# Optimization experiments

Hardware: AMD Instinct MI355X
Metric: run time of the kernel (lower is better)

## Reference

```python
import jax, jax.numpy as jnp
import numpy as np

N_NODES = 50000
N_EDGES = 100000
N_RELS = 64
D_IN = 64
D_OUT = 64


def setup_inputs() -> dict:
    key = jax.random.key(0)
    k1, k2, k3, k4, k5, k6 = jax.random.split(key, 6)
    h = jax.random.normal(k1, (N_NODES, D_IN), dtype=jnp.float32)
    src = jax.random.randint(k2, (N_EDGES,), 0, N_NODES)
    rel = jax.random.randint(k3, (N_EDGES,), 0, N_RELS)
    dst = jax.random.randint(k4, (N_EDGES,), 0, N_NODES)
    edges = jnp.stack([src, rel, dst], axis=1)
    # xavier_uniform with gain for relu: bound = gain * sqrt(6 / (fan_in + fan_out))
    gain = float(np.sqrt(2.0))
    bound = gain * float(np.sqrt(6.0 / (D_IN + D_OUT)))
    weight = jax.random.uniform(k5, (N_RELS, D_IN, D_OUT), dtype=jnp.float32,
                                minval=-bound, maxval=bound)
    self_loop_weight = jax.random.uniform(k6, (D_IN, D_OUT), dtype=jnp.float32,
                                          minval=-bound, maxval=bound)
    return {"h": h, "edges": edges, "weight": weight,
            "self_loop_weight": self_loop_weight}


def reference(h, edges, weight, self_loop_weight):
    # h: (N, D_IN); edges: (E, 3) int columns (src, rel, dst)
    src, rel, dst = edges[:, 0], edges[:, 1], edges[:, 2]
    n_nodes = h.shape[0]
    n_edges = src.shape[0]

    # per-edge relation-specific transform: (E,1,in) bmm (E,in,out) -> (E,out)
    src_h = h[src]                                    # (E, D_IN)
    msg = jnp.einsum('ei,eio->eo', src_h, weight[rel])  # (E, D_OUT)

    # -> last edge index per destination node
    last_edge = jax.ops.segment_max(jnp.arange(n_edges, dtype=jnp.int32), dst,
                                    num_segments=n_nodes)  # (N,)
    # msg = msg[index_matrix[dst]]: every edge to node d takes the msg of the
    # last edge pointing to d
    msg = msg[last_edge[dst]]                          # (E, D_OUT)

    # scatter-mean aggregate over dst (only nodes with incoming edges updated)
    sums = jax.ops.segment_sum(msg, dst, num_segments=n_nodes)          # (N, D_OUT)
    counts = jax.ops.segment_sum(jnp.ones((n_edges,), h.dtype), dst,
                                 num_segments=n_nodes)                   # (N,)
    has_in = counts > 0
    agg = jnp.where(has_in[:, None],
                    sums / jnp.maximum(counts, 1.0)[:, None], 0.0)

    out = h @ self_loop_weight                         # (N, D_OUT)
    return out + agg
```

## Files before the change

### kernel.cpp

```cpp
#include <hip/hip_runtime.h>

#define NN 50000
#define NE 100000
#define NREL 64
#define D 64
#define RCAP 1280
#define SCAP 8192
#define CSTR 16
#define BR   8
#define SBLK 64
#define FILL_BLOCKS 128
#define FILL_ITERS  2

#define SC_BLK ((NE + 255) / 256)
#define TR_BLK 65
#define HC_BLK 160

typedef unsigned long long u64;
using f16x8 = __attribute__((ext_vector_type(8))) _Float16;
using f32x4 = __attribute__((ext_vector_type(4))) float;

#define WS_CURSOR  (400 * 1024)
#define WS_RBUCKET (408 * 1024)
#define WS_SBUCKET (736 * 1024)
#define WS_H2      (768 * 1024)
#define WS_WST     (7168 * 1024)
#define WS_W16T    (7176 * 1024)

struct H4 { _Float16 v[4]; };

__global__ __launch_bounds__(256) void k_init(u64* __restrict__ packed, int* __restrict__ cursor) {
    const int t = blockIdx.x * 256 + threadIdx.x;
    const int nthr = gridDim.x * 256;
    for (int i = t; i < NN; i += nthr) packed[i] = 0ull;
    if (t < 65) cursor[t * CSTR] = 0;
}

__global__ __launch_bounds__(256) void k_scatpre(
    const int* __restrict__ edges, const float* __restrict__ h,
    const float* __restrict__ weight, const float* __restrict__ wself,
    u64* __restrict__ packed, _Float16* __restrict__ h2,
    _Float16* __restrict__ w16T, _Float16* __restrict__ wsT)
{
    __shared__ _Float16 tile[D * D];

    if (blockIdx.x < SC_BLK) {
        const int e = blockIdx.x * 256 + threadIdx.x;
        if (e < NE) {
            const int s = edges[e * 3 + 0];
            const int r = edges[e * 3 + 1];
            const int d = edges[e * 3 + 2];
            const u64 key = ((u64)(e + 1) << 22) | ((u64)r << 16) | (u64)s;
            atomicMax(&packed[d], key);
        }
        return;
    }

    if (blockIdx.x < SC_BLK + TR_BLK) {
        const int r = blockIdx.x - SC_BLK;
        const float4* __restrict__ src4 = reinterpret_cast<const float4*>(
            (r < NREL) ? (weight + (size_t)r * D * D) : wself);
        #pragma unroll
        for (int it = 0; it < 4; ++it) {
            const int idx = it * 256 + threadIdx.x;
            const float4 w = src4[idx];
            const int k  = idx >> 4;
            const int n0 = (idx & 15) << 2;
            tile[(n0 + 0) * D + k] = (_Float16)w.x;
            tile[(n0 + 1) * D + k] = (_Float16)w.y;
            tile[(n0 + 2) * D + k] = (_Float16)w.z;
            tile[(n0 + 3) * D + k] = (_Float16)w.w;
        }
        __syncthreads();
        f16x8* __restrict__ dst = reinterpret_cast<f16x8*>(
            (r < NREL) ? (w16T + ((size_t)r << 12)) : wsT);
        const f16x8* __restrict__ src = reinterpret_cast<const f16x8*>(tile);
        #pragma unroll
        for (int it = 0; it < 2; ++it)
            dst[it * 256 + threadIdx.x] = src[it * 256 + threadIdx.x];
        return;
    }

    const int t = (blockIdx.x - SC_BLK - TR_BLK) * 256 + threadIdx.x;
    const int nthr = HC_BLK * 256;
    const float4* __restrict__ hf4 = reinterpret_cast<const float4*>(h);
    H4* __restrict__ o4 = reinterpret_cast<H4*>(h2);
    for (int m = t; m < NN * (D / 4); m += nthr) {
        const float4 p = hf4[m];
        H4 o;
        o.v[0] = (_Float16)p.x; o.v[1] = (_Float16)p.y;
        o.v[2] = (_Float16)p.z; o.v[3] = (_Float16)p.w;
        o4[m] = o;
    }
}

__global__ __launch_bounds__(256) void k_fill(
    const u64* __restrict__ packed, int* __restrict__ cursor,
    unsigned* __restrict__ rbucket, unsigned* __restrict__ sbucket)
{
    __shared__ int hcnt[65];
    __shared__ int hbase[65];
    const int t = threadIdx.x;
    if (t < 65) hcnt[t] = 0;
    __syncthreads();

    int      myr[FILL_ITERS];
    int      myslot[FILL_ITERS];
    unsigned myent[FILL_ITERS];

    #pragma unroll
    for (int it = 0; it < FILL_ITERS; ++it) {
        const int v = (blockIdx.x * FILL_ITERS + it) * 256 + t;
        myr[it] = -1;
        if (v < NN) {
            u64 key = packed[v];
            if (key) {
                myr[it]   = (int)((key >> 16) & 63);
                myent[it] = ((unsigned)v << 16) | (unsigned)(key & 0xFFFF);
            } else {
                myr[it]   = 64;
                myent[it] = (unsigned)v;
            }
            myslot[it] = atomicAdd(&hcnt[myr[it]], 1);
        }
    }
    __syncthreads();
    if (t < 65 && hcnt[t] > 0)
        hbase[t] = atomicAdd(&cursor[t * CSTR], hcnt[t]);
    __syncthreads();

    #pragma unroll
    for (int it = 0; it < FILL_ITERS; ++it) {
        const int r = myr[it];
        if (r >= 0) {
            const int p = hbase[r] + myslot[it];
            if (r < 64) { if (p < RCAP) rbucket[r * RCAP + p] = myent[it]; }
            else        { if (p < SCAP) sbucket[p] = myent[it]; }
        }
    }
}

__global__ __launch_bounds__(256) void k_compute(
    const _Float16* __restrict__ h2, const _Float16* __restrict__ w16T,
    const _Float16* __restrict__ wsT, const unsigned* __restrict__ rbucket,
    const unsigned* __restrict__ sbucket, const int* __restrict__ cursor,
    float* __restrict__ out)
{
    const int lane = threadIdx.x & 63;
    const int wv   = threadIdx.x >> 6;
    const bool isRel = blockIdx.x < NREL * BR;

    int r = 64, wslot, wstride, cnt;
    const unsigned* __restrict__ seg;
    if (isRel) {
        r = blockIdx.x / BR;
        wslot = (blockIdx.x % BR) * 4 + wv;
        wstride = BR * 4;
        seg = rbucket + r * RCAP;
        cnt = min(cursor[r * CSTR], RCAP);
    } else {
        wslot = (blockIdx.x - NREL * BR) * 4 + wv;
        wstride = SBLK * 4;
        seg = sbucket;
        cnt = min(cursor[64 * CSTR], SCAP);
    }
    if (cnt == 0 || wslot * 16 >= cnt) return;

    const int kbase = (lane >> 4) * 8;
    const int ncol  = lane & 15;

    f16x8 was[4][2];
    #pragma unroll
    for (int nt = 0; nt < 4; ++nt)
        #pragma unroll
        for (int ks = 0; ks < 2; ++ks)
            was[nt][ks] = *reinterpret_cast<const f16x8*>(
                wsT + (size_t)(nt * 16 + ncol) * D + ks * 32 + kbase);

    f16x8 wa[4][2];
    if (isRel) {
        const _Float16* __restrict__ wr = w16T + ((size_t)r << 12);
        #pragma unroll
        for (int nt = 0; nt < 4; ++nt)
            #pragma unroll
            for (int ks = 0; ks < 2; ++ks)
                wa[nt][ks] = *reinterpret_cast<const f16x8*>(
                    wr + (size_t)(nt * 16 + ncol) * D + ks * 32 + kbase);
    }

    for (int t = wslot; t * 16 < cnt; t += wstride) {
        const unsigned ent = seg[min(t * 16 + ncol, cnt - 1)];
        const int v = isRel ? (int)(ent >> 16) : (int)ent;
        const int s = (int)(ent & 0xFFFF);

        f32x4 c[4];
        #pragma unroll
        for (int nt = 0; nt < 4; ++nt) c[nt] = (f32x4){0.f, 0.f, 0.f, 0.f};

        {
            const f16x8 b0 = *reinterpret_cast<const f16x8*>(h2 + (size_t)v * D + kbase);
            const f16x8 b1 = *reinterpret_cast<const f16x8*>(h2 + (size_t)v * D + 32 + kbase);
            #pragma unroll
            for (int nt = 0; nt < 4; ++nt) {
                c[nt] = __builtin_amdgcn_mfma_f32_16x16x32_f16(was[nt][0], b0, c[nt], 0, 0, 0);
                c[nt] = __builtin_amdgcn_mfma_f32_16x16x32_f16(was[nt][1], b1, c[nt], 0, 0, 0);
            }
        }
        if (isRel) {
            const f16x8 b0 = *reinterpret_cast<const f16x8*>(h2 + (size_t)s * D + kbase);
            const f16x8 b1 = *reinterpret_cast<const f16x8*>(h2 + (size_t)s * D + 32 + kbase);
            #pragma unroll
            for (int nt = 0; nt < 4; ++nt) {
                c[nt] = __builtin_amdgcn_mfma_f32_16x16x32_f16(wa[nt][0], b0, c[nt], 0, 0, 0);
                c[nt] = __builtin_amdgcn_mfma_f32_16x16x32_f16(wa[nt][1], b1, c[nt], 0, 0, 0);
            }
        }

        float* __restrict__ orow = out + (size_t)v * D + (lane >> 4) * 4;
        #pragma unroll
        for (int nt = 0; nt < 4; ++nt) {
            *reinterpret_cast<float4*>(orow + nt * 16) =
                make_float4(c[nt][0], c[nt][1], c[nt][2], c[nt][3]);
        }
    }
}

extern "C" void kernel_launch(void* const* d_in, const int* in_sizes, int n_in,
                              void* d_out, int out_size, void* d_ws, size_t ws_size,
                              hipStream_t stream) {
    const float* h      = (const float*)d_in[0];
    const int*   edges  = (const int*)d_in[1];
    const float* weight = (const float*)d_in[2];
    const float* wself  = (const float*)d_in[3];
    float* out = (float*)d_out;

    char* ws = (char*)d_ws;
    u64*      packed  = (u64*)ws;
    int*      cursor  = (int*)(ws + WS_CURSOR);
    unsigned* rbucket = (unsigned*)(ws + WS_RBUCKET);
    unsigned* sbucket = (unsigned*)(ws + WS_SBUCKET);
    _Float16* h2      = (_Float16*)(ws + WS_H2);
    _Float16* wsT     = (_Float16*)(ws + WS_WST);
    _Float16* w16T    = (_Float16*)(ws + WS_W16T);

    k_init<<<98, 256, 0, stream>>>(packed, cursor);
    k_scatpre<<<SC_BLK + TR_BLK + HC_BLK, 256, 0, stream>>>(
        edges, h, weight, wself, packed, h2, w16T, wsT);
    k_fill<<<FILL_BLOCKS, 256, 0, stream>>>(packed, cursor, rbucket, sbucket);
    k_compute<<<NREL * BR + SBLK, 256, 0, stream>>>(h2, w16T, wsT, rbucket, sbucket, cursor, out);
}
```

Baseline: 39.94 us.

## Fold init into preprocessing kernel and split edge scatter into its own launch

```diff
diff --git a/kernel.cpp b/kernel.cpp
--- a/kernel.cpp
+++ b/kernel.cpp
@@ -11,10 +11,7 @@
 #define SBLK 64
 #define FILL_BLOCKS 128
 #define FILL_ITERS  2
-
-#define SC_BLK ((NE + 255) / 256)
-#define TR_BLK 65
-#define HC_BLK 160
+#define PRE_BLOCKS 512
 
 typedef unsigned long long u64;
 using f16x8 = __attribute__((ext_vector_type(8))) _Float16;
@@ -29,40 +26,28 @@
 
 struct H4 { _Float16 v[4]; };
 
-__global__ __launch_bounds__(256) void k_init(u64* __restrict__ packed, int* __restrict__ cursor) {
-    const int t = blockIdx.x * 256 + threadIdx.x;
-    const int nthr = gridDim.x * 256;
-    for (int i = t; i < NN; i += nthr) packed[i] = 0ull;
-    if (t < 65) cursor[t * CSTR] = 0;
-}
-
-__global__ __launch_bounds__(256) void k_scatpre(
-    const int* __restrict__ edges, const float* __restrict__ h,
-    const float* __restrict__ weight, const float* __restrict__ wself,
-    u64* __restrict__ packed, _Float16* __restrict__ h2,
+__global__ __launch_bounds__(256) void k_pre(
+    const float* __restrict__ h, const float* __restrict__ weight,
+    const float* __restrict__ wself, u64* __restrict__ packed,
+    int* __restrict__ cursor, _Float16* __restrict__ h2,
     _Float16* __restrict__ w16T, _Float16* __restrict__ wsT)
 {
     __shared__ _Float16 tile[D * D];
 
-    if (blockIdx.x < SC_BLK) {
-        const int e = blockIdx.x * 256 + threadIdx.x;
-        if (e < NE) {
-            const int s = edges[e * 3 + 0];
-            const int r = edges[e * 3 + 1];
-            const int d = edges[e * 3 + 2];
-            const u64 key = ((u64)(e + 1) << 22) | ((u64)r << 16) | (u64)s;
-            atomicMax(&packed[d], key);
-        }
-        return;
-    }
-
-    if (blockIdx.x < SC_BLK + TR_BLK) {
-        const int r = blockIdx.x - SC_BLK;
+    const int b = blockIdx.x;
+    const int t = threadIdx.x;
+    const int gt = b * 256 + t;
+    const int nthr = PRE_BLOCKS * 256;
+
+    for (int i = gt; i < NN; i += nthr) packed[i] = 0ull;
+    if (gt < 65) cursor[gt * CSTR] = 0;
+
+    if (b < 65) {
         const float4* __restrict__ src4 = reinterpret_cast<const float4*>(
-            (r < NREL) ? (weight + (size_t)r * D * D) : wself);
+            (b < NREL) ? (weight + (size_t)b * D * D) : wself);
         #pragma unroll
         for (int it = 0; it < 4; ++it) {
-            const int idx = it * 256 + threadIdx.x;
+            const int idx = it * 256 + t;
             const float4 w = src4[idx];
             const int k  = idx >> 4;
             const int n0 = (idx & 15) << 2;
@@ -73,24 +58,32 @@
         }
         __syncthreads();
         f16x8* __restrict__ dst = reinterpret_cast<f16x8*>(
-            (r < NREL) ? (w16T + ((size_t)r << 12)) : wsT);
+            (b < NREL) ? (w16T + ((size_t)b << 12)) : wsT);
         const f16x8* __restrict__ src = reinterpret_cast<const f16x8*>(tile);
         #pragma unroll
         for (int it = 0; it < 2; ++it)
-            dst[it * 256 + threadIdx.x] = src[it * 256 + threadIdx.x];
-        return;
-    }
-
-    const int t = (blockIdx.x - SC_BLK - TR_BLK) * 256 + threadIdx.x;
-    const int nthr = HC_BLK * 256;
+            dst[it * 256 + t] = src[it * 256 + t];
+    }
+
     const float4* __restrict__ hf4 = reinterpret_cast<const float4*>(h);
     H4* __restrict__ o4 = reinterpret_cast<H4*>(h2);
-    for (int m = t; m < NN * (D / 4); m += nthr) {
+    for (int m = gt; m < NN * (D / 4); m += nthr) {
         const float4 p = hf4[m];
         H4 o;
         o.v[0] = (_Float16)p.x; o.v[1] = (_Float16)p.y;
         o.v[2] = (_Float16)p.z; o.v[3] = (_Float16)p.w;
         o4[m] = o;
+    }
+}
+
+__global__ void k_scatter(const int* __restrict__ edges, u64* __restrict__ packed) {
+    int e = blockIdx.x * blockDim.x + threadIdx.x;
+    if (e < NE) {
+        int s = edges[e * 3 + 0];
+        int r = edges[e * 3 + 1];
+        int d = edges[e * 3 + 2];
+        u64 key = ((u64)(e + 1) << 22) | ((u64)r << 16) | (u64)s;
+        atomicMax(&packed[d], key);
     }
 }
 
@@ -188,8 +181,8 @@
                     wr + (size_t)(nt * 16 + ncol) * D + ks * 32 + kbase);
     }
 
-    for (int t = wslot; t * 16 < cnt; t += wstride) {
-        const unsigned ent = seg[min(t * 16 + ncol, cnt - 1)];
+    for (int tt = wslot; tt * 16 < cnt; tt += wstride) {
+        const unsigned ent = seg[min(tt * 16 + ncol, cnt - 1)];
         const int v = isRel ? (int)(ent >> 16) : (int)ent;
         const int s = (int)(ent & 0xFFFF);
 
@@ -218,10 +211,9 @@
 
         float* __restrict__ orow = out + (size_t)v * D + (lane >> 4) * 4;
         #pragma unroll
-        for (int nt = 0; nt < 4; ++nt) {
+        for (int nt = 0; nt < 4; ++nt)
             *reinterpret_cast<float4*>(orow + nt * 16) =
                 make_float4(c[nt][0], c[nt][1], c[nt][2], c[nt][3]);
-        }
     }
 }
 
@@ -243,9 +235,8 @@
     _Float16* wsT     = (_Float16*)(ws + WS_WST);
     _Float16* w16T    = (_Float16*)(ws + WS_W16T);
 
-    k_init<<<98, 256, 0, stream>>>(packed, cursor);
-    k_scatpre<<<SC_BLK + TR_BLK + HC_BLK, 256, 0, stream>>>(
-        edges, h, weight, wself, packed, h2, w16T, wsT);
+    k_pre<<<PRE_BLOCKS, 256, 0, stream>>>(h, weight, wself, packed, cursor, h2, w16T, wsT);
+    k_scatter<<<(NE + 255) / 256, 256, 0, stream>>>(edges, packed);
     k_fill<<<FILL_BLOCKS, 256, 0, stream>>>(packed, cursor, rbucket, sbucket);
     k_compute<<<NREL * BR + SBLK, 256, 0, stream>>>(h2, w16T, wsT, rbucket, sbucket, cursor, out);
 }
```

Measured after the change: 35.43 us. -11.3%, faster.

## Convert h to fp16 inside compute kernel and drop separate h conversion pass

Applied to the files above, without the earlier changes.

```diff
diff --git a/kernel.cpp b/kernel.cpp
--- a/kernel.cpp
+++ b/kernel.cpp
@@ -7,14 +7,12 @@
 #define RCAP 1280
 #define SCAP 8192
 #define CSTR 16
-#define BR   8
+#define BR   12
 #define SBLK 64
 #define FILL_BLOCKS 128
 #define FILL_ITERS  2
-
 #define SC_BLK ((NE + 255) / 256)
 #define TR_BLK 65
-#define HC_BLK 160
 
 typedef unsigned long long u64;
 using f16x8 = __attribute__((ext_vector_type(8))) _Float16;
@@ -23,23 +21,19 @@
 #define WS_CURSOR  (400 * 1024)
 #define WS_RBUCKET (408 * 1024)
 #define WS_SBUCKET (736 * 1024)
-#define WS_H2      (768 * 1024)
-#define WS_WST     (7168 * 1024)
-#define WS_W16T    (7176 * 1024)
-
-struct H4 { _Float16 v[4]; };
-
-__global__ __launch_bounds__(256) void k_init(u64* __restrict__ packed, int* __restrict__ cursor) {
-    const int t = blockIdx.x * 256 + threadIdx.x;
+#define WS_WST     (768 * 1024)
+#define WS_W16T    (776 * 1024)
+
+__global__ __launch_bounds__(256) void k_zero(u64* __restrict__ packed, int* __restrict__ cursor) {
+    const int gt = blockIdx.x * 256 + threadIdx.x;
     const int nthr = gridDim.x * 256;
-    for (int i = t; i < NN; i += nthr) packed[i] = 0ull;
-    if (t < 65) cursor[t * CSTR] = 0;
-}
-
-__global__ __launch_bounds__(256) void k_scatpre(
-    const int* __restrict__ edges, const float* __restrict__ h,
-    const float* __restrict__ weight, const float* __restrict__ wself,
-    u64* __restrict__ packed, _Float16* __restrict__ h2,
+    for (int i = gt; i < NN; i += nthr) packed[i] = 0ull;
+    if (gt < 65) cursor[gt * CSTR] = 0;
+}
+
+__global__ __launch_bounds__(256) void k_scatter(
+    const int* __restrict__ edges, const float* __restrict__ weight,
+    const float* __restrict__ wself, u64* __restrict__ packed,
     _Float16* __restrict__ w16T, _Float16* __restrict__ wsT)
 {
     __shared__ _Float16 tile[D * D];
@@ -56,42 +50,28 @@
         return;
     }
 
-    if (blockIdx.x < SC_BLK + TR_BLK) {
-        const int r = blockIdx.x - SC_BLK;
-        const float4* __restrict__ src4 = reinterpret_cast<const float4*>(
-            (r < NREL) ? (weight + (size_t)r * D * D) : wself);
-        #pragma unroll
-        for (int it = 0; it < 4; ++it) {
-            const int idx = it * 256 + threadIdx.x;
-            const float4 w = src4[idx];
-            const int k  = idx >> 4;
-            const int n0 = (idx & 15) << 2;
-            tile[(n0 + 0) * D + k] = (_Float16)w.x;
-            tile[(n0 + 1) * D + k] = (_Float16)w.y;
-            tile[(n0 + 2) * D + k] = (_Float16)w.z;
-            tile[(n0 + 3) * D + k] = (_Float16)w.w;
-        }
-        __syncthreads();
-        f16x8* __restrict__ dst = reinterpret_cast<f16x8*>(
-            (r < NREL) ? (w16T + ((size_t)r << 12)) : wsT);
-        const f16x8* __restrict__ src = reinterpret_cast<const f16x8*>(tile);
-        #pragma unroll
-        for (int it = 0; it < 2; ++it)
-            dst[it * 256 + threadIdx.x] = src[it * 256 + threadIdx.x];
-        return;
-    }
-
-    const int t = (blockIdx.x - SC_BLK - TR_BLK) * 256 + threadIdx.x;
-    const int nthr = HC_BLK * 256;
-    const float4* __restrict__ hf4 = reinterpret_cast<const float4*>(h);
-    H4* __restrict__ o4 = reinterpret_cast<H4*>(h2);
-    for (int m = t; m < NN * (D / 4); m += nthr) {
-        const float4 p = hf4[m];
-        H4 o;
-        o.v[0] = (_Float16)p.x; o.v[1] = (_Float16)p.y;
-        o.v[2] = (_Float16)p.z; o.v[3] = (_Float16)p.w;
-        o4[m] = o;
-    }
+    const int r = blockIdx.x - SC_BLK;
+    const int t = threadIdx.x;
+    const float4* __restrict__ src4 = reinterpret_cast<const float4*>(
+        (r < NREL) ? (weight + (size_t)r * D * D) : wself);
+    #pragma unroll
+    for (int it = 0; it < 4; ++it) {
+        const int idx = it * 256 + t;
+        const float4 w = src4[idx];
+        const int k  = idx >> 4;
+        const int n0 = (idx & 15) << 2;
+        tile[(n0 + 0) * D + k] = (_Float16)w.x;
+        tile[(n0 + 1) * D + k] = (_Float16)w.y;
+        tile[(n0 + 2) * D + k] = (_Float16)w.z;
+        tile[(n0 + 3) * D + k] = (_Float16)w.w;
+    }
+    __syncthreads();
+    f16x8* __restrict__ dst = reinterpret_cast<f16x8*>(
+        (r < NREL) ? (w16T + ((size_t)r << 12)) : wsT);
+    const f16x8* __restrict__ src = reinterpret_cast<const f16x8*>(tile);
+    #pragma unroll
+    for (int it = 0; it < 2; ++it)
+        dst[it * 256 + t] = src[it * 256 + t];
 }
 
 __global__ __launch_bounds__(256) void k_fill(
@@ -113,7 +93,7 @@
         const int v = (blockIdx.x * FILL_ITERS + it) * 256 + t;
         myr[it] = -1;
         if (v < NN) {
-            u64 key = packed[v];
+            const u64 key = packed[v];
             if (key) {
                 myr[it]   = (int)((key >> 16) & 63);
                 myent[it] = ((unsigned)v << 16) | (unsigned)(key & 0xFFFF);
@@ -140,8 +120,17 @@
     }
 }
 
+__device__ __forceinline__ f16x8 cvt_frag(const float* __restrict__ p) {
+    const float4 p0 = *reinterpret_cast<const float4*>(p);
+    const float4 p1 = *reinterpret_cast<const float4*>(p + 4);
+    f16x8 a;
+    a[0] = (_Float16)p0.x; a[1] = (_Float16)p0.y; a[2] = (_Float16)p0.z; a[3] = (_Float16)p0.w;
+    a[4] = (_Float16)p1.x; a[5] = (_Float16)p1.y; a[6] = (_Float16)p1.z; a[7] = (_Float16)p1.w;
+    return a;
+}
+
 __global__ __launch_bounds__(256) void k_compute(
-    const _Float16* __restrict__ h2, const _Float16* __restrict__ w16T,
+    const float* __restrict__ h, const _Float16* __restrict__ w16T,
     const _Float16* __restrict__ wsT, const unsigned* __restrict__ rbucket,
     const unsigned* __restrict__ sbucket, const int* __restrict__ cursor,
     float* __restrict__ out)
@@ -169,22 +158,22 @@
     const int kbase = (lane >> 4) * 8;
     const int ncol  = lane & 15;
 
-    f16x8 was[4][2];
+    f16x8 bws[4][2];
     #pragma unroll
     for (int nt = 0; nt < 4; ++nt)
         #pragma unroll
         for (int ks = 0; ks < 2; ++ks)
-            was[nt][ks] = *reinterpret_cast<const f16x8*>(
+            bws[nt][ks] = *reinterpret_cast<const f16x8*>(
                 wsT + (size_t)(nt * 16 + ncol) * D + ks * 32 + kbase);
 
-    f16x8 wa[4][2];
+    f16x8 bw[4][2];
     if (isRel) {
         const _Float16* __restrict__ wr = w16T + ((size_t)r << 12);
         #pragma unroll
         for (int nt = 0; nt < 4; ++nt)
             #pragma unroll
             for (int ks = 0; ks < 2; ++ks)
-                wa[nt][ks] = *reinterpret_cast<const f16x8*>(
+                bw[nt][ks] = *reinterpret_cast<const f16x8*>(
                     wr + (size_t)(nt * 16 + ncol) * D + ks * 32 + kbase);
     }
 
@@ -193,35 +182,43 @@
         const int v = isRel ? (int)(ent >> 16) : (int)ent;
         const int s = (int)(ent & 0xFFFF);
 
+        const float* __restrict__ hv = h + (size_t)v * D;
+        const f16x8 a0 = cvt_frag(hv + kbase);
+        const f16x8 a1 = cvt_frag(hv + 32 + kbase);
+
         f32x4 c[4];
         #pragma unroll
         for (int nt = 0; nt < 4; ++nt) c[nt] = (f32x4){0.f, 0.f, 0.f, 0.f};
 
-        {
-            const f16x8 b0 = *reinterpret_cast<const f16x8*>(h2 + (size_t)v * D + kbase);
-            const f16x8 b1 = *reinterpret_cast<const f16x8*>(h2 + (size_t)v * D + 32 + kbase);
+        if (isRel) {
+            const float* __restrict__ hs = h + (size_t)s * D;
+            const f16x8 b0 = cvt_frag(hs + kbase);
+            const f16x8 b1 = cvt_frag(hs + 32 + kbase);
             #pragma unroll
             for (int nt = 0; nt < 4; ++nt) {
-                c[nt] = __builtin_amdgcn_mfma_f32_16x16x32_f16(was[nt][0], b0, c[nt], 0, 0, 0);
-                c[nt] = __builtin_amdgcn_mfma_f32_16x16x32_f16(was[nt][1], b1, c[nt], 0, 0, 0);
+                c[nt] = __builtin_amdgcn_mfma_f32_16x16x32_f16(a0, bws[nt][0], c[nt], 0, 0, 0);
+                c[nt] = __builtin_amdgcn_mfma_f32_16x16x32_f16(a1, bws[nt][1], c[nt], 0, 0, 0);
+                c[nt] = __builtin_amdgcn_mfma_f32_16x16x32_f16(b0, bw[nt][0], c[nt], 0, 0, 0);
+                c[nt] = __builtin_amdgcn_mfma_f32_16x16x32_f16(b1, bw[nt][1], c[nt], 0, 0, 0);
             }
-        }
-        if (isRel) {
-            const f16x8 b0 = *reinterpret_cast<const f16x8*>(h2 + (size_t)s * D + kbase);
-            const f16x8 b1 = *reinterpret_cast<const f16x8*>(h2 + (size_t)s * D + 32 + kbase);
+        } else {
             #pragma unroll
             for (int nt = 0; nt < 4; ++nt) {
-                c[nt] = __builtin_amdgcn_mfma_f32_16x16x32_f16(wa[nt][0], b0, c[nt], 0, 0, 0);
-                c[nt] = __builtin_amdgcn_mfma_f32_16x16x32_f16(wa[nt][1], b1, c[nt], 0, 0, 0);
+                c[nt] = __builtin_amdgcn_mfma_f32_16x16x32_f16(a0, bws[nt][0], c[nt], 0, 0, 0);
+                c[nt] = __builtin_amdgcn_mfma_f32_16x16x32_f16(a1, bws[nt][1], c[nt], 0, 0, 0);
             }
         }
 
-        float* __restrict__ orow = out + (size_t)v * D + (lane >> 4) * 4;
-        #pragma unroll
-        for (int nt = 0; nt < 4; ++nt) {
-            *reinterpret_cast<float4*>(orow + nt * 16) =
-                make_float4(c[nt][0], c[nt][1], c[nt][2], c[nt][3]);
-        }
+        int vrow[4];
+        #pragma unroll
+        for (int q = 0; q < 4; ++q)
+            vrow[q] = __shfl(v, (lane >> 4) * 4 + q, 64);
+
+        #pragma unroll
+        for (int nt = 0; nt < 4; ++nt)
+            #pragma unroll
+            for (int q = 0; q < 4; ++q)
+                out[(size_t)vrow[q] * D + nt * 16 + ncol] = c[nt][q];
     }
 }
 
@@ -239,13 +236,11 @@
     int*      cursor  = (int*)(ws + WS_CURSOR);
     unsigned* rbucket = (unsigned*)(ws + WS_RBUCKET);
     unsigned* sbucket = (unsigned*)(ws + WS_SBUCKET);
-    _Float16* h2      = (_Float16*)(ws + WS_H2);
     _Float16* wsT     = (_Float16*)(ws + WS_WST);
     _Float16* w16T    = (_Float16*)(ws + WS_W16T);
 
-    k_init<<<98, 256, 0, stream>>>(packed, cursor);
-    k_scatpre<<<SC_BLK + TR_BLK + HC_BLK, 256, 0, stream>>>(
-        edges, h, weight, wself, packed, h2, w16T, wsT);
+    k_zero<<<98, 256, 0, stream>>>(packed, cursor);
+    k_scatter<<<SC_BLK + TR_BLK, 256, 0, stream>>>(edges, weight, wself, packed, w16T, wsT);
     k_fill<<<FILL_BLOCKS, 256, 0, stream>>>(packed, cursor, rbucket, sbucket);
-    k_compute<<<NREL * BR + SBLK, 256, 0, stream>>>(h2, w16T, wsT, rbucket, sbucket, cursor, out);
-}
+    k_compute<<<NREL * BR + SBLK, 256, 0, stream>>>(h, w16T, wsT, rbucket, sbucket, cursor, out);
+}
```

Result: faster. 34.54 us (-13.5%).
